# Kernel optimization log

Hardware: AMD Instinct MI355X
Metric: run time of the kernel (lower is better)

Reference implementation:

```python
import jax, jax.numpy as jnp
import numpy as np

B, S, E, D = 8, 2048, 512, 512  # batch, seq (mesh edges), elem_size, embd_size


def setup_inputs() -> dict:
    key = jax.random.key(0)
    ks = jax.random.split(key, 5)
    scale = 1.0 / np.sqrt(E)
    return {
        "x": jax.random.normal(ks[0], (B, S, E), dtype=jnp.float32),
        "Wq": jax.random.normal(ks[1], (E, D), dtype=jnp.float32) * scale,
        "bq": jax.random.normal(ks[2], (D,), dtype=jnp.float32) * 0.01,
        "Wk": jax.random.normal(ks[3], (E, D), dtype=jnp.float32) * scale,
        "bk": jax.random.normal(ks[4], (D,), dtype=jnp.float32) * 0.01,
    }


def reference(x, Wq, bq, Wk, bk):
    elem_size = x.shape[-1]
    q = jax.nn.relu(x @ Wq + bq)              # [B,S,D]
    k = jax.nn.relu(x @ Wk + bk)              # [B,S,D]
    scores = jnp.einsum("bqd,bkd->bqk", q, k) / (elem_size ** 0.5)  # [B,S,S]
    # nn.Softmax(dim=1): normalize over the QUERY axis (column-wise softmax)
    attn = jax.nn.softmax(scores, axis=1)
    new_values = jnp.einsum("bqk,bke->bqe", attn, x)  # V = raw x (use_V=False)
    return x + new_values                     # residual connection
```

## Files before the change

### kernel.cpp

```cpp
#include <hip/hip_runtime.h>
#include <hip/hip_bf16.h>
#include <math.h>

#define Bb 8
#define Ss 2048
#define Ee 512
#define Dd 512
#define QSPLIT 16

typedef __bf16 bf16x8 __attribute__((ext_vector_type(8)));
typedef __bf16 bf16x4 __attribute__((ext_vector_type(4)));
typedef float f32x4 __attribute__((ext_vector_type(4)));

__device__ __forceinline__ void stage_async(ushort* lds, const __bf16* gbase,
                                            int ldg, int wave, int lane) {
#pragma unroll
    for (int t = 0; t < 2; ++t) {
        const int idx = wave * 2 + t;
        const int row = idx * 16 + (lane >> 2);
        const int q8  = (((lane & 3) ^ ((lane >> 3) & 3)) * 8);
        __builtin_amdgcn_global_load_lds(
            (const __attribute__((address_space(1))) void*)(gbase + (size_t)row * ldg + q8),
            (__attribute__((address_space(3))) void*)(lds + idx * 512),
            16, 0, 0);
    }
}

__global__ void prep_x(const float* __restrict__ in, __bf16* __restrict__ xb,
                       __bf16* __restrict__ xT) {
    __shared__ float tile[32][33];
    const int b  = blockIdx.z;
    const int e0 = blockIdx.x * 32;
    const int s0 = blockIdx.y * 32;
    const float* ip = in + (size_t)b * Ss * Ee;
    __bf16* xbp = xb + (size_t)b * Ss * Ee;
    __bf16* xTp = xT + (size_t)b * Ee * Ss;
    for (int i = threadIdx.y; i < 32; i += 8) {
        const float v = ip[(size_t)(s0 + i) * Ee + e0 + threadIdx.x];
        tile[i][threadIdx.x] = v;
        xbp[(size_t)(s0 + i) * Ee + e0 + threadIdx.x] = (__bf16)v;
    }
    __syncthreads();
    for (int i = threadIdx.y; i < 32; i += 8)
        xTp[(size_t)(e0 + i) * Ss + s0 + threadIdx.x] = (__bf16)tile[threadIdx.x][i];
}

__global__ void transpose_w(const float* __restrict__ Wq, const float* __restrict__ Wk,
                            __bf16* __restrict__ WqT, __bf16* __restrict__ WkT) {
    __shared__ float tile[32][33];
    const float* in = blockIdx.z ? Wk : Wq;
    __bf16* out = blockIdx.z ? WkT : WqT;
    const int x0 = blockIdx.x * 32;
    const int y0 = blockIdx.y * 32;
    for (int i = threadIdx.y; i < 32; i += 8)
        tile[i][threadIdx.x] = in[(size_t)(y0 + i) * 512 + (x0 + threadIdx.x)];
    __syncthreads();
    for (int i = threadIdx.y; i < 32; i += 8)
        out[(size_t)(x0 + i) * 512 + (y0 + threadIdx.x)] = (__bf16)tile[threadIdx.x][i];
}

__global__ __launch_bounds__(256, 4) void proj_kernel(
    const __bf16* __restrict__ X,
    const __bf16* __restrict__ WqT, const __bf16* __restrict__ WkT,
    const float* __restrict__ bq, const float* __restrict__ bk,
    __bf16* __restrict__ qb, __bf16* __restrict__ kb)
{
    __shared__ __align__(16) ushort As[128 * 32];
    __shared__ __align__(16) ushort Bs[128 * 32];
    const __bf16* WT  = blockIdx.z ? WkT : WqT;
    const float* bias = blockIdx.z ? bk : bq;
    __bf16* Out       = blockIdx.z ? kb : qb;

    const int tid = threadIdx.x;
    const int wave = tid >> 6, lane = tid & 63, quad = lane >> 4, l16 = lane & 15;
    const int wm = (wave >> 1) * 64, wn = (wave & 1) * 64;
    const int m0 = blockIdx.y * 128, n0 = blockIdx.x * 128;
    const int sw = (quad ^ ((l16 >> 1) & 3)) * 8;
    const int K = 512;

    f32x4 acc[4][4];
    f32x4 zero = {0.f, 0.f, 0.f, 0.f};
    for (int i = 0; i < 4; i++) for (int j = 0; j < 4; j++) acc[i][j] = zero;

    for (int k0 = 0; k0 < K; k0 += 32) {
        stage_async(As, X  + (size_t)m0 * K + k0, K, wave, lane);
        stage_async(Bs, WT + (size_t)n0 * K + k0, K, wave, lane);
        __syncthreads();
        bf16x8 af[4], bfr[4];
        for (int i = 0; i < 4; i++) af[i]  = *(bf16x8*)&As[(wm + i * 16 + l16) * 32 + sw];
        for (int j = 0; j < 4; j++) bfr[j] = *(bf16x8*)&Bs[(wn + j * 16 + l16) * 32 + sw];
        for (int i = 0; i < 4; i++)
            for (int j = 0; j < 4; j++)
                acc[i][j] = __builtin_amdgcn_mfma_f32_16x16x32_bf16(af[i], bfr[j], acc[i][j], 0, 0, 0);
        __syncthreads();
    }

    for (int i = 0; i < 4; i++) {
        const int row = m0 + wm + i * 16 + quad * 4;
        for (int j = 0; j < 4; j++) {
            const int col = n0 + wn + j * 16 + l16;
            const float bv = bias[col];
            for (int rr = 0; rr < 4; rr++) {
                float v = acc[i][j][rr] + bv;
                v = v > 0.f ? v : 0.f;
                Out[(size_t)(row + rr) * 512 + col] = (__bf16)v;
            }
        }
    }
}

__global__ __launch_bounds__(256, 4) void scores_kernel(
    const __bf16* __restrict__ Q,
    const __bf16* __restrict__ Km,
    __bf16* __restrict__ P,
    float* __restrict__ Mp,
    float* __restrict__ Lp)
{
    __shared__ __align__(16) ushort As[128 * 32];
    __shared__ __align__(16) ushort Bs[128 * 32];
    const int id = blockIdx.x;
    const int b = id & 7;
    const int rest = id >> 3;
    const int qy = rest >> 4;
    const int m0 = qy * 128;
    const int n0 = (rest & 15) * 128;
    const __bf16* A  = Q  + (size_t)b * Ss * Dd;
    const __bf16* Bp = Km + (size_t)b * Ss * Dd;
    __bf16* C = P + (size_t)b * Ss * Ss;

    const int tid = threadIdx.x;
    const int wave = tid >> 6, lane = tid & 63, quad = lane >> 4, l16 = lane & 15;
    const int wm = (wave >> 1) * 64, wn = (wave & 1) * 64;
    const int sw = (quad ^ ((l16 >> 1) & 3)) * 8;
    const float scale = 0.044194173824159216f;

    f32x4 acc[4][4];
    f32x4 zero = {0.f, 0.f, 0.f, 0.f};
    for (int i = 0; i < 4; i++) for (int j = 0; j < 4; j++) acc[i][j] = zero;

    for (int k0 = 0; k0 < Dd; k0 += 32) {
        stage_async(As, A  + (size_t)m0 * Dd + k0, Dd, wave, lane);
        stage_async(Bs, Bp + (size_t)n0 * Dd + k0, Dd, wave, lane);
        __syncthreads();
        bf16x8 af[4], bfr[4];
        for (int i = 0; i < 4; i++) af[i]  = *(bf16x8*)&As[(wm + i * 16 + l16) * 32 + sw];
        for (int j = 0; j < 4; j++) bfr[j] = *(bf16x8*)&Bs[(wn + j * 16 + l16) * 32 + sw];
        for (int i = 0; i < 4; i++)
            for (int j = 0; j < 4; j++)
                acc[i][j] = __builtin_amdgcn_mfma_f32_16x16x32_bf16(af[i], bfr[j], acc[i][j], 0, 0, 0);
        __syncthreads();
    }

    float* Ms = (float*)As;
    float* Ls = ((float*)As) + 256;
    const int half = wave >> 1;
    float mj[4];
    for (int j = 0; j < 4; j++) {
        float m = -1e30f;
        for (int i = 0; i < 4; i++)
            for (int rr = 0; rr < 4; rr++)
                m = fmaxf(m, acc[i][j][rr]);
        m = fmaxf(m, __shfl_xor(m, 16));
        m = fmaxf(m, __shfl_xor(m, 32));
        mj[j] = m;
    }
    if (quad == 0)
        for (int j = 0; j < 4; j++) Ms[half * 128 + wn + j * 16 + l16] = mj[j];
    __syncthreads();
    float mt[4];
    for (int j = 0; j < 4; j++) {
        const int c = wn + j * 16 + l16;
        mt[j] = fmaxf(Ms[c], Ms[128 + c]);
    }
    float lj[4];
    for (int j = 0; j < 4; j++) {
        const int col = n0 + wn + j * 16 + l16;
        float l = 0.f;
        for (int i = 0; i < 4; i++) {
            const int row = m0 + wm + i * 16 + quad * 4;
            for (int rr = 0; rr < 4; rr++) {
                const float e = __expf((acc[i][j][rr] - mt[j]) * scale);
                C[(size_t)(row + rr) * Ss + col] = (__bf16)e;
                l += e;
            }
        }
        l += __shfl_xor(l, 16);
        l += __shfl_xor(l, 32);
        lj[j] = l;
    }
    if (quad == 0)
        for (int j = 0; j < 4; j++) Ls[half * 128 + wn + j * 16 + l16] = lj[j];
    __syncthreads();
    if (tid < 128) {
        const size_t o = ((size_t)qy * Bb + b) * Ss + n0 + tid;
        Mp[o] = fmaxf(Ms[tid], Ms[128 + tid]) * scale;
        Lp[o] = Ls[tid] + Ls[128 + tid];
    }
}

__global__ void stats_combine(const float* __restrict__ Mp, const float* __restrict__ Lp,
                              float* __restrict__ Mf, float* __restrict__ Li) {
    const int idx = blockIdx.x * 256 + threadIdx.x;
    float m = -1e30f;
    for (int qy = 0; qy < QSPLIT; qy++) m = fmaxf(m, Mp[(size_t)qy * Bb * Ss + idx]);
    float l = 0.f;
    for (int qy = 0; qy < QSPLIT; qy++)
        l += Lp[(size_t)qy * Bb * Ss + idx] * __expf(Mp[(size_t)qy * Bb * Ss + idx] - m);
    Mf[idx] = m;
    Li[idx] = 1.0f / l;
}

__global__ __launch_bounds__(256, 4) void pv_kernel(
    const __bf16* __restrict__ P,
    const float* __restrict__ Mp,
    const float* __restrict__ Mf,
    const float* __restrict__ Li,
    const __bf16* __restrict__ XT,
    const __bf16* __restrict__ XB,
    float* __restrict__ Out)
{
    __shared__ __align__(16) ushort As[128 * 32];
    __shared__ __align__(16) ushort Bs[128 * 32];
    __shared__ float corr[Ss];
    const int id = blockIdx.x;
    const int b = id & 7;
    const int rest = id >> 3;
    const int qy = rest >> 2;
    const int m0 = qy * 128;
    const int n0 = (rest & 3) * 128;
    const __bf16* A  = P  + (size_t)b * Ss * Ss;
    const __bf16* Bp = XT + (size_t)b * Ee * Ss;

    const int tid = threadIdx.x;
    const int wave = tid >> 6, lane = tid & 63, quad = lane >> 4, l16 = lane & 15;
    const int wm = (wave >> 1) * 64, wn = (wave & 1) * 64;
    const int sw = (quad ^ ((l16 >> 1) & 3)) * 8;
    const int r = tid >> 2, seg = (tid & 3) * 8;
    const int p8 = (((tid & 3) ^ ((r >> 1) & 3)) * 8);

    for (int k = tid; k < Ss; k += 256) {
        const float mp = Mp[((size_t)qy * Bb + b) * Ss + k];
        corr[k] = __expf(mp - Mf[(size_t)b * Ss + k]) * Li[(size_t)b * Ss + k];
    }
    __syncthreads();

    f32x4 acc[4][4];
    f32x4 zero = {0.f, 0.f, 0.f, 0.f};
    for (int i = 0; i < 4; i++) for (int j = 0; j < 4; j++) acc[i][j] = zero;

    const __bf16* Arow0 = A + (size_t)(m0 + r) * Ss;
    const __bf16* Arow1 = A + (size_t)(m0 + r + 64) * Ss;
    bf16x8 pr0 = *(const bf16x8*)&Arow0[seg];
    bf16x8 pr1 = *(const bf16x8*)&Arow1[seg];

    for (int k0 = 0; k0 < Ss; k0 += 32) {
        stage_async(Bs, Bp + (size_t)n0 * Ss + k0, Ss, wave, lane);
        float cv[8];
        #pragma unroll
        for (int t = 0; t < 8; t++) cv[t] = corr[k0 + seg + t];
        bf16x8 o0, o1;
        #pragma unroll
        for (int t = 0; t < 8; t++) o0[t] = (__bf16)((float)pr0[t] * cv[t]);
        #pragma unroll
        for (int t = 0; t < 8; t++) o1[t] = (__bf16)((float)pr1[t] * cv[t]);
        *(bf16x8*)&As[r * 32 + p8]        = o0;
        *(bf16x8*)&As[(r + 64) * 32 + p8] = o1;
        __syncthreads();
        bf16x8 af[4], bfr[4];
        for (int i = 0; i < 4; i++) af[i]  = *(bf16x8*)&As[(wm + i * 16 + l16) * 32 + sw];
        for (int j = 0; j < 4; j++) bfr[j] = *(bf16x8*)&Bs[(wn + j * 16 + l16) * 32 + sw];
        const int kn = (k0 + 32) & (Ss - 1);
        pr0 = *(const bf16x8*)&Arow0[kn + seg];
        pr1 = *(const bf16x8*)&Arow1[kn + seg];
        for (int i = 0; i < 4; i++)
            for (int j = 0; j < 4; j++)
                acc[i][j] = __builtin_amdgcn_mfma_f32_16x16x32_bf16(af[i], bfr[j], acc[i][j], 0, 0, 0);
        __syncthreads();
    }

    for (int i = 0; i < 4; i++) {
        const int row = m0 + wm + i * 16 + quad * 4;
        for (int j = 0; j < 4; j++) {
            const int col = wn + j * 16 + l16 + n0;
            for (int rr = 0; rr < 4; rr++) {
                const size_t idx = ((size_t)b * Ss + row + rr) * Ee + col;
                Out[idx] = (float)XB[idx] + acc[i][j][rr];
            }
        }
    }
}

extern "C" void kernel_launch(void* const* d_in, const int* in_sizes, int n_in,
                              void* d_out, int out_size, void* d_ws, size_t ws_size,
                              hipStream_t stream) {
    const float* x  = (const float*)d_in[0];
    const float* Wq = (const float*)d_in[1];
    const float* bq = (const float*)d_in[2];
    const float* Wk = (const float*)d_in[3];
    const float* bk = (const float*)d_in[4];
    float* out = (float*)d_out;

    char* ws = (char*)d_ws;
    size_t off = 0;
    auto alloc = [&](size_t bytes) -> void* {
        void* p = ws + off;
        off += (bytes + 255) & ~(size_t)255;
        return p;
    };
    __bf16* P   = (__bf16*)alloc((size_t)Bb * Ss * Ss * 2);
    __bf16* xb  = (__bf16*)alloc((size_t)Bb * Ss * Ee * 2);
    __bf16* qb  = (__bf16*)alloc((size_t)Bb * Ss * Dd * 2);
    __bf16* kb  = (__bf16*)alloc((size_t)Bb * Ss * Dd * 2);
    __bf16* xT  = (__bf16*)alloc((size_t)Bb * Ee * Ss * 2);
    __bf16* WqT = (__bf16*)alloc((size_t)512 * 512 * 2);
    __bf16* WkT = (__bf16*)alloc((size_t)512 * 512 * 2);
    float*  Mp  = (float*)alloc((size_t)QSPLIT * Bb * Ss * 4);
    float*  Lp  = (float*)alloc((size_t)QSPLIT * Bb * Ss * 4);
    float*  Mf  = (float*)alloc((size_t)Bb * Ss * 4);
    float*  Li  = (float*)alloc((size_t)Bb * Ss * 4);
    if (off > ws_size) return;

    prep_x<<<dim3(16, 64, 8), dim3(32, 8), 0, stream>>>(x, xb, xT);
    transpose_w<<<dim3(16, 16, 2), dim3(32, 8), 0, stream>>>(Wq, Wk, WqT, WkT);

    proj_kernel<<<dim3(4, 128, 2), 256, 0, stream>>>(xb, WqT, WkT, bq, bk, qb, kb);

    scores_kernel<<<dim3(2048), 256, 0, stream>>>(qb, kb, P, Mp, Lp);
    stats_combine<<<dim3(Bb * Ss / 256), 256, 0, stream>>>(Mp, Lp, Mf, Li);

    pv_kernel<<<dim3(512), 256, 0, stream>>>(P, Mp, Mf, Li, xT, xb, out);
}
```

Measured before the change: 232.2 us.

## Precompute per-split softmax correction and halve PV tile rows for more blocks

stats_combine now writes a per-query-split correction factor (exp(Mp - m) / l) for every column, so pv_kernel no longer builds a 2048-entry correction table in LDS at block start. Instead it streams the correction values from global memory alongside the P rows. pv_kernel switches to 64x128 tiles with 128 threads (two waves) and 1024 blocks, which raises block count and reduces LDS per block. The cost is that each block reloads the same B tile, so XT traffic doubles, and there is an extra global read stream for the correction values.

```diff
diff --git a/kernel.cpp b/kernel.cpp
--- a/kernel.cpp
+++ b/kernel.cpp
@@ -17,6 +17,20 @@
 #pragma unroll
     for (int t = 0; t < 2; ++t) {
         const int idx = wave * 2 + t;
+        const int row = idx * 16 + (lane >> 2);
+        const int q8  = (((lane & 3) ^ ((lane >> 3) & 3)) * 8);
+        __builtin_amdgcn_global_load_lds(
+            (const __attribute__((address_space(1))) void*)(gbase + (size_t)row * ldg + q8),
+            (__attribute__((address_space(3))) void*)(lds + idx * 512),
+            16, 0, 0);
+    }
+}
+
+__device__ __forceinline__ void stage_async2(ushort* lds, const __bf16* gbase,
+                                             int ldg, int wave, int lane) {
+#pragma unroll
+    for (int t = 0; t < 4; ++t) {
+        const int idx = wave * 4 + t;
         const int row = idx * 16 + (lane >> 2);
         const int q8  = (((lane & 3) ^ ((lane >> 3) & 3)) * 8);
         __builtin_amdgcn_global_load_lds(
@@ -199,79 +213,76 @@
 }
 
 __global__ void stats_combine(const float* __restrict__ Mp, const float* __restrict__ Lp,
-                              float* __restrict__ Mf, float* __restrict__ Li) {
+                              float* __restrict__ Corr) {
     const int idx = blockIdx.x * 256 + threadIdx.x;
     float m = -1e30f;
     for (int qy = 0; qy < QSPLIT; qy++) m = fmaxf(m, Mp[(size_t)qy * Bb * Ss + idx]);
     float l = 0.f;
     for (int qy = 0; qy < QSPLIT; qy++)
         l += Lp[(size_t)qy * Bb * Ss + idx] * __expf(Mp[(size_t)qy * Bb * Ss + idx] - m);
-    Mf[idx] = m;
-    Li[idx] = 1.0f / l;
-}
-
-__global__ __launch_bounds__(256, 4) void pv_kernel(
+    const float li = 1.0f / l;
+    for (int qy = 0; qy < QSPLIT; qy++)
+        Corr[(size_t)qy * Bb * Ss + idx] = __expf(Mp[(size_t)qy * Bb * Ss + idx] - m) * li;
+}
+
+__global__ __launch_bounds__(128, 2) void pv_kernel(
     const __bf16* __restrict__ P,
-    const float* __restrict__ Mp,
-    const float* __restrict__ Mf,
-    const float* __restrict__ Li,
+    const float* __restrict__ Corr,
     const __bf16* __restrict__ XT,
     const __bf16* __restrict__ XB,
     float* __restrict__ Out)
 {
-    __shared__ __align__(16) ushort As[128 * 32];
+    __shared__ __align__(16) ushort As[64 * 32];
     __shared__ __align__(16) ushort Bs[128 * 32];
-    __shared__ float corr[Ss];
     const int id = blockIdx.x;
     const int b = id & 7;
     const int rest = id >> 3;
-    const int qy = rest >> 2;
-    const int m0 = qy * 128;
+    const int m0 = (rest >> 2) * 64;
     const int n0 = (rest & 3) * 128;
+    const int qy = m0 >> 7;
     const __bf16* A  = P  + (size_t)b * Ss * Ss;
     const __bf16* Bp = XT + (size_t)b * Ee * Ss;
+    const float* Cr  = Corr + ((size_t)qy * Bb + b) * Ss;
 
     const int tid = threadIdx.x;
     const int wave = tid >> 6, lane = tid & 63, quad = lane >> 4, l16 = lane & 15;
-    const int wm = (wave >> 1) * 64, wn = (wave & 1) * 64;
+    const int wn = wave * 64;
     const int sw = (quad ^ ((l16 >> 1) & 3)) * 8;
     const int r = tid >> 2, seg = (tid & 3) * 8;
     const int p8 = (((tid & 3) ^ ((r >> 1) & 3)) * 8);
 
-    for (int k = tid; k < Ss; k += 256) {
-        const float mp = Mp[((size_t)qy * Bb + b) * Ss + k];
-        corr[k] = __expf(mp - Mf[(size_t)b * Ss + k]) * Li[(size_t)b * Ss + k];
-    }
-    __syncthreads();
-
     f32x4 acc[4][4];
     f32x4 zero = {0.f, 0.f, 0.f, 0.f};
     for (int i = 0; i < 4; i++) for (int j = 0; j < 4; j++) acc[i][j] = zero;
 
     const __bf16* Arow0 = A + (size_t)(m0 + r) * Ss;
-    const __bf16* Arow1 = A + (size_t)(m0 + r + 64) * Ss;
+    const __bf16* Arow1 = A + (size_t)(m0 + r + 32) * Ss;
     bf16x8 pr0 = *(const bf16x8*)&Arow0[seg];
     bf16x8 pr1 = *(const bf16x8*)&Arow1[seg];
+    float4 cra = *(const float4*)&Cr[seg];
+    float4 crb = *(const float4*)&Cr[seg + 4];
 
     for (int k0 = 0; k0 < Ss; k0 += 32) {
-        stage_async(Bs, Bp + (size_t)n0 * Ss + k0, Ss, wave, lane);
+        stage_async2(Bs, Bp + (size_t)n0 * Ss + k0, Ss, wave, lane);
         float cv[8];
-        #pragma unroll
-        for (int t = 0; t < 8; t++) cv[t] = corr[k0 + seg + t];
+        cv[0] = cra.x; cv[1] = cra.y; cv[2] = cra.z; cv[3] = cra.w;
+        cv[4] = crb.x; cv[5] = crb.y; cv[6] = crb.z; cv[7] = crb.w;
         bf16x8 o0, o1;
         #pragma unroll
         for (int t = 0; t < 8; t++) o0[t] = (__bf16)((float)pr0[t] * cv[t]);
         #pragma unroll
         for (int t = 0; t < 8; t++) o1[t] = (__bf16)((float)pr1[t] * cv[t]);
         *(bf16x8*)&As[r * 32 + p8]        = o0;
-        *(bf16x8*)&As[(r + 64) * 32 + p8] = o1;
+        *(bf16x8*)&As[(r + 32) * 32 + p8] = o1;
         __syncthreads();
         bf16x8 af[4], bfr[4];
-        for (int i = 0; i < 4; i++) af[i]  = *(bf16x8*)&As[(wm + i * 16 + l16) * 32 + sw];
+        for (int i = 0; i < 4; i++) af[i]  = *(bf16x8*)&As[(i * 16 + l16) * 32 + sw];
         for (int j = 0; j < 4; j++) bfr[j] = *(bf16x8*)&Bs[(wn + j * 16 + l16) * 32 + sw];
         const int kn = (k0 + 32) & (Ss - 1);
         pr0 = *(const bf16x8*)&Arow0[kn + seg];
         pr1 = *(const bf16x8*)&Arow1[kn + seg];
+        cra = *(const float4*)&Cr[kn + seg];
+        crb = *(const float4*)&Cr[kn + seg + 4];
         for (int i = 0; i < 4; i++)
             for (int j = 0; j < 4; j++)
                 acc[i][j] = __builtin_amdgcn_mfma_f32_16x16x32_bf16(af[i], bfr[j], acc[i][j], 0, 0, 0);
@@ -279,9 +290,9 @@
     }
 
     for (int i = 0; i < 4; i++) {
-        const int row = m0 + wm + i * 16 + quad * 4;
+        const int row = m0 + i * 16 + quad * 4;
         for (int j = 0; j < 4; j++) {
-            const int col = wn + j * 16 + l16 + n0;
+            const int col = n0 + wn + j * 16 + l16;
             for (int rr = 0; rr < 4; rr++) {
                 const size_t idx = ((size_t)b * Ss + row + rr) * Ee + col;
                 Out[idx] = (float)XB[idx] + acc[i][j][rr];
@@ -307,17 +318,16 @@
         off += (bytes + 255) & ~(size_t)255;
         return p;
     };
-    __bf16* P   = (__bf16*)alloc((size_t)Bb * Ss * Ss * 2);
-    __bf16* xb  = (__bf16*)alloc((size_t)Bb * Ss * Ee * 2);
-    __bf16* qb  = (__bf16*)alloc((size_t)Bb * Ss * Dd * 2);
-    __bf16* kb  = (__bf16*)alloc((size_t)Bb * Ss * Dd * 2);
-    __bf16* xT  = (__bf16*)alloc((size_t)Bb * Ee * Ss * 2);
-    __bf16* WqT = (__bf16*)alloc((size_t)512 * 512 * 2);
-    __bf16* WkT = (__bf16*)alloc((size_t)512 * 512 * 2);
-    float*  Mp  = (float*)alloc((size_t)QSPLIT * Bb * Ss * 4);
-    float*  Lp  = (float*)alloc((size_t)QSPLIT * Bb * Ss * 4);
-    float*  Mf  = (float*)alloc((size_t)Bb * Ss * 4);
-    float*  Li  = (float*)alloc((size_t)Bb * Ss * 4);
+    __bf16* P    = (__bf16*)alloc((size_t)Bb * Ss * Ss * 2);
+    __bf16* xb   = (__bf16*)alloc((size_t)Bb * Ss * Ee * 2);
+    __bf16* qb   = (__bf16*)alloc((size_t)Bb * Ss * Dd * 2);
+    __bf16* kb   = (__bf16*)alloc((size_t)Bb * Ss * Dd * 2);
+    __bf16* xT   = (__bf16*)alloc((size_t)Bb * Ee * Ss * 2);
+    __bf16* WqT  = (__bf16*)alloc((size_t)512 * 512 * 2);
+    __bf16* WkT  = (__bf16*)alloc((size_t)512 * 512 * 2);
+    float*  Mp   = (float*)alloc((size_t)QSPLIT * Bb * Ss * 4);
+    float*  Lp   = (float*)alloc((size_t)QSPLIT * Bb * Ss * 4);
+    float*  Corr = (float*)alloc((size_t)QSPLIT * Bb * Ss * 4);
     if (off > ws_size) return;
 
     prep_x<<<dim3(16, 64, 8), dim3(32, 8), 0, stream>>>(x, xb, xT);
@@ -326,7 +336,7 @@
     proj_kernel<<<dim3(4, 128, 2), 256, 0, stream>>>(xb, WqT, WkT, bq, bk, qb, kb);
 
     scores_kernel<<<dim3(2048), 256, 0, stream>>>(qb, kb, P, Mp, Lp);
-    stats_combine<<<dim3(Bb * Ss / 256), 256, 0, stream>>>(Mp, Lp, Mf, Li);
-
-    pv_kernel<<<dim3(512), 256, 0, stream>>>(P, Mp, Mf, Li, xT, xb, out);
-}
+    stats_combine<<<dim3(Bb * Ss / 256), 256, 0, stream>>>(Mp, Lp, Corr);
+
+    pv_kernel<<<dim3(1024), 128, 0, stream>>>(P, Corr, xT, xb, out);
+}
```

Result: no change. 232.7 us (+0.2%).
